# Kernel optimization log

Hardware: AMD Instinct MI355X
Metric: run time of the kernel (lower is better)

Reference implementation:

```python
import jax, jax.numpy as jnp
import numpy as np

DIM = 4096
N_HEADS = 32
N_KV_HEADS = 8
HEAD_DIM = 128
EPS = 1e-6
B, S = 1, 2048


def setup_inputs() -> dict:
    key = jax.random.key(0)
    ks = jax.random.split(key, 8)
    x = jax.random.normal(ks[0], (B, S, DIM), dtype=jnp.float32)
    # Standard RoPE cos/sin table, broadcast to (B, S, HEAD_DIM)
    inv_freq = 1.0 / (10000.0 ** (np.arange(0, HEAD_DIM, 2, dtype=np.float32) / HEAD_DIM))
    t = np.arange(S, dtype=np.float32)
    freqs = np.outer(t, inv_freq)  # (S, HEAD_DIM/2)
    emb = np.concatenate([freqs, freqs], axis=-1)  # (S, HEAD_DIM)
    cos = jnp.broadcast_to(jnp.cos(emb)[None], (B, S, HEAD_DIM))
    sin = jnp.broadcast_to(jnp.sin(emb)[None], (B, S, HEAD_DIM))
    std = 0.02
    wq = jax.random.normal(ks[1], (N_HEADS * HEAD_DIM, DIM), dtype=jnp.float32) * std
    wk = jax.random.normal(ks[2], (N_KV_HEADS * HEAD_DIM, DIM), dtype=jnp.float32) * std
    wv = jax.random.normal(ks[3], (N_KV_HEADS * HEAD_DIM, DIM), dtype=jnp.float32) * std
    wo = jax.random.normal(ks[4], (DIM, N_HEADS * HEAD_DIM), dtype=jnp.float32) * std
    q_norm_w = jnp.ones((HEAD_DIM,), dtype=jnp.float32) + 0.1 * jax.random.normal(ks[5], (HEAD_DIM,), dtype=jnp.float32)
    k_norm_w = jnp.ones((HEAD_DIM,), dtype=jnp.float32) + 0.1 * jax.random.normal(ks[6], (HEAD_DIM,), dtype=jnp.float32)
    return {"x": x, "cos": cos, "sin": sin, "wq": wq, "wk": wk, "wv": wv,
            "wo": wo, "q_norm_w": q_norm_w, "k_norm_w": k_norm_w}


def _rmsnorm(x, w):
    var = jnp.mean(jnp.square(x), axis=-1, keepdims=True)
    return x * jax.lax.rsqrt(var + EPS) * w


def _rotate_half(x):
    h = x.shape[-1] // 2
    return jnp.concatenate([-x[..., h:], x[..., :h]], axis=-1)


def reference(x, cos, sin, wq, wk, wv, wo, q_norm_w, k_norm_w):
    bs, seqlen, _ = x.shape
    # QKV projections (Linear with weight of shape (out, in), no bias)
    xq = (x @ wq.T).reshape(bs, seqlen, N_HEADS, HEAD_DIM)
    xk = (x @ wk.T).reshape(bs, seqlen, N_KV_HEADS, HEAD_DIM)
    xv = (x @ wv.T).reshape(bs, seqlen, N_KV_HEADS, HEAD_DIM)
    # QK RMSNorm (after projection, before RoPE)
    xq = _rmsnorm(xq, q_norm_w)
    xk = _rmsnorm(xk, k_norm_w)
    # RoPE: cos/sin (B, S, D) -> broadcast over head axis
    c = cos[:, :, None, :]
    s = sin[:, :, None, :]
    xq = xq * c + _rotate_half(xq) * s
    xk = xk * c + _rotate_half(xk) * s
    # GQA: repeat kv heads
    n_rep = N_HEADS // N_KV_HEADS
    xk = jnp.repeat(xk, n_rep, axis=2)
    xv = jnp.repeat(xv, n_rep, axis=2)
    # (B, H, S, D)
    q = xq.transpose(0, 2, 1, 3)
    k = xk.transpose(0, 2, 1, 3)
    v = xv.transpose(0, 2, 1, 3)
    scale = HEAD_DIM ** -0.5
    scores = jnp.einsum('bhqd,bhkd->bhqk', q, k) * scale
    causal = jnp.tril(jnp.ones((seqlen, seqlen), dtype=bool))
    scores = jnp.where(causal, scores, jnp.finfo(scores.dtype).min)
    probs = jax.nn.softmax(scores, axis=-1)
    out = jnp.einsum('bhqk,bhkd->bhqd', probs, v)
    out = out.transpose(0, 2, 1, 3).reshape(bs, seqlen, N_HEADS * HEAD_DIM)
    return out @ wo.T
```

## Files before the change

### kernel.cpp

```cpp
#include <hip/hip_runtime.h>


#define S_LEN 2048
#define DIM 4096
#define NH 32
#define NKV 8
#define HD 128
#define SCALE 0.08838834764831845f

typedef __attribute__((ext_vector_type(8))) short short8;
typedef __attribute__((ext_vector_type(4))) float f32x4;

__device__ __forceinline__ float bf2f(unsigned short u) {
  union { unsigned i; float f; } c; c.i = ((unsigned)u) << 16; return c.f;
}
__device__ __forceinline__ unsigned short f2bf(float f) {
  union { float f; unsigned u; } c; c.f = f;
  return (unsigned short)((c.u + 0x7fffu + ((c.u >> 16) & 1u)) >> 16);
}
__device__ __forceinline__ void cvt8(const float* __restrict__ g,
                                     unsigned short* __restrict__ d) {
  const float4 a = *(const float4*)g;
  const float4 b = *(const float4*)(g + 4);
  short8 p;
  p[0] = (short)f2bf(a.x); p[1] = (short)f2bf(a.y);
  p[2] = (short)f2bf(a.z); p[3] = (short)f2bf(a.w);
  p[4] = (short)f2bf(b.x); p[5] = (short)f2bf(b.y);
  p[6] = (short)f2bf(b.z); p[7] = (short)f2bf(b.w);
  *(short8*)d = p;
}
__device__ __forceinline__ void storeC(float* p, float v) { *p = v; }
__device__ __forceinline__ void storeC(unsigned short* p, float v) { *p = f2bf(v); }

#define G_X   1048576u
#define G_WQ  2097152u
#define G_WK   524288u
#define G_WV   524288u
#define G_QKV (G_WQ + G_WK + G_WV)

__global__ __launch_bounds__(256)
void cvt_all(const float* __restrict__ x,  const float* __restrict__ wq,
             const float* __restrict__ wk, const float* __restrict__ wv,
             const float* __restrict__ wo,
             unsigned short* __restrict__ xb,
             unsigned short* __restrict__ wqkvb,
             unsigned short* __restrict__ wob) {
  const size_t g = (size_t)blockIdx.x * 256 + threadIdx.x;
  if (g < G_X) {
    cvt8(x + g * 8, xb + g * 8);
  } else if (g < G_X + G_QKV) {
    const size_t o = g - G_X;
    const float* s = (o < G_WQ) ? wq + o * 8
                   : (o < G_WQ + G_WK) ? wk + (o - G_WQ) * 8
                                       : wv + (o - G_WQ - G_WK) * 8;
    cvt8(s, wqkvb + o * 8);
  } else {
    const size_t o = g - (G_X + G_QKV);
    cvt8(wo + o * 8, wob + o * 8);
  }
}

template <int QKV, typename TC>
__global__ __launch_bounds__(256)
void gemm16(const unsigned short* __restrict__ A,
            const unsigned short* __restrict__ B,
            TC* __restrict__ C0,
            unsigned short* __restrict__ Ck,
            unsigned short* __restrict__ Cv, int K) {
  __shared__ unsigned short lsA[128 * 64];
  __shared__ unsigned short lsB[128 * 64];

  const int t    = threadIdx.x;
  const int lane = t & 63;
  const int w    = t >> 6;
  const int m0   = blockIdx.y * 128;
  const int n0   = blockIdx.x * 128;

  f32x4 acc[4][4];
#pragma unroll
  for (int a = 0; a < 4; ++a)
#pragma unroll
    for (int b = 0; b < 4; ++b)
#pragma unroll
      for (int e = 0; e < 4; ++e) acc[a][b][e] = 0.f;

  const int l15  = lane & 15;
  const int qd   = lane >> 4;
  const int wr   = w >> 1, wc = w & 1;
  const int sr8  = lane >> 3;
  const int skg  = (lane & 7) ^ sr8;
  const int l7   = l15 & 7;

  const int nkb = K >> 6;
  for (int kb = 0; kb < nkb; ++kb) {
    const int k0 = kb << 6;
#pragma unroll
    for (int c = 0; c < 4; ++c) {
      const int chunk = c * 4 + w;
      const int row   = chunk * 8 + sr8;
      const unsigned short* ga = A + (size_t)(m0 + row) * K + k0 + skg * 8;
      const unsigned short* gb = B + (size_t)(n0 + row) * K + k0 + skg * 8;
      __builtin_amdgcn_global_load_lds(
          (const __attribute__((address_space(1))) void*)ga,
          (__attribute__((address_space(3))) void*)(lsA + chunk * 512), 16, 0, 0);
      __builtin_amdgcn_global_load_lds(
          (const __attribute__((address_space(1))) void*)gb,
          (__attribute__((address_space(3))) void*)(lsB + chunk * 512), 16, 0, 0);
    }
    asm volatile("s_waitcnt vmcnt(0)" ::: "memory");
    __syncthreads();

#pragma unroll
    for (int half = 0; half < 2; ++half) {
      const int kg = (half * 4 + qd) ^ l7;
      short8 af[4], bf[4];
#pragma unroll
      for (int mi = 0; mi < 4; ++mi)
        af[mi] = *(const short8*)(lsA + (wr * 64 + mi * 16 + l15) * 64 + kg * 8);
#pragma unroll
      for (int ni = 0; ni < 4; ++ni)
        bf[ni] = *(const short8*)(lsB + (wc * 64 + ni * 16 + l15) * 64 + kg * 8);
#pragma unroll
      for (int mi = 0; mi < 4; ++mi)
#pragma unroll
        for (int ni = 0; ni < 4; ++ni)
          acc[mi][ni] = __builtin_amdgcn_mfma_f32_16x16x32_bf16(
              af[mi], bf[ni], acc[mi][ni], 0, 0, 0);
    }
    __syncthreads();
  }

#pragma unroll
  for (int mi = 0; mi < 4; ++mi)
#pragma unroll
    for (int i = 0; i < 4; ++i) {
      const int grow = m0 + wr * 64 + mi * 16 + qd * 4 + i;
#pragma unroll
      for (int ni = 0; ni < 4; ++ni) {
        const int gcol = n0 + wc * 64 + ni * 16 + l15;
        if (QKV) {
          if (n0 < 4096)
            storeC((unsigned short*)C0 + (size_t)grow * 4096 + gcol,
                   acc[mi][ni][i]);
          else if (n0 < 5120)
            Ck[(size_t)grow * 1024 + (gcol - 4096)] = f2bf(acc[mi][ni][i]);
          else
            Cv[(size_t)(gcol - 5120) * S_LEN + grow] = f2bf(acc[mi][ni][i]);
        } else {
          storeC(C0 + (size_t)grow * 4096 + gcol, acc[mi][ni][i]);
        }
      }
    }
}

__global__ __launch_bounds__(512)
void norm_rope(unsigned short* __restrict__ qb, unsigned short* __restrict__ kb,
               const float* __restrict__ cosb, const float* __restrict__ sinb,
               const float* __restrict__ qw, const float* __restrict__ kw) {
  const int s    = blockIdx.x;
  const int w    = threadIdx.x >> 6;
  const int l    = threadIdx.x & 63;
  const int hh   = blockIdx.y * 8 + w;

  unsigned short* p; const float* wt;
  if (hh < NH) { p = qb + (size_t)s * (NH * HD) + hh * HD; wt = qw; }
  else         { p = kb + (size_t)s * (NKV * HD) + (hh - NH) * HD; wt = kw; }

  const float v0 = bf2f(p[l]);
  const float v1 = bf2f(p[l + 64]);
  float ss = v0 * v0 + v1 * v1;
#pragma unroll
  for (int off = 32; off; off >>= 1) ss += __shfl_xor(ss, off);
  const float r = rsqrtf(ss * (1.f / 128.f) + 1e-6f);

  const float xn0 = v0 * r * wt[l];
  const float xn1 = v1 * r * wt[l + 64];
  const float c0 = cosb[s * HD + l],      s0 = sinb[s * HD + l];
  const float c1 = cosb[s * HD + l + 64], s1 = sinb[s * HD + l + 64];
  float o0 = xn0 * c0 - xn1 * s0;
  float o1 = xn1 * c1 + xn0 * s1;
  if (hh < NH) { o0 *= SCALE; o1 *= SCALE; }
  p[l]      = f2bf(o0);
  p[l + 64] = f2bf(o1);
}

#define PSTR 72

__global__ __launch_bounds__(256)
void attn_mfma(const unsigned short* __restrict__ qB,
               const unsigned short* __restrict__ kB,
               const unsigned short* __restrict__ vT,
               unsigned short* __restrict__ oB) {
  __shared__ unsigned short ks[64 * 128];
  __shared__ unsigned short vt[128 * 64];
  __shared__ unsigned short Ps[4 * 32 * PSTR];

  const int t    = threadIdx.x;
  const int lane = t & 63;
  const int w    = t >> 6;
  const int h    = blockIdx.y;
  const int qt   = (h & 16) ? (15 - blockIdx.x) : blockIdx.x;
  const int q0   = qt * 128;
  const int kvh  = h >> 2;
  const int l15  = lane & 15;
  const int qd   = lane >> 4;
  const int l7   = l15 & 7;

  const int kr16 = lane >> 4;
  const int vr8  = lane >> 3;
  const int vkg  = (lane & 7) ^ (vr8 & 7);

  short8 qf[2][4];
#pragma unroll
  for (int f = 0; f < 2; ++f) {
    const unsigned short* qp =
        qB + (size_t)(q0 + w * 32 + f * 16 + l15) * (NH * HD) + h * HD + qd * 8;
#pragma unroll
    for (int s = 0; s < 4; ++s) qf[f][s] = *(const short8*)(qp + s * 32);
  }

  f32x4 O[2][8];
#pragma unroll
  for (int f = 0; f < 2; ++f)
#pragma unroll
    for (int nt = 0; nt < 8; ++nt)
#pragma unroll
      for (int e = 0; e < 4; ++e) O[f][nt][e] = 0.f;
  float l_i[2][4] = {{0.f, 0.f, 0.f, 0.f}, {0.f, 0.f, 0.f, 0.f}};

  unsigned short* Pw = Ps + w * (32 * PSTR);

  const int nkt = 2 * qt + 2;
  for (int kt = 0; kt < nkt; ++kt) {
#pragma unroll
    for (int c = 0; c < 4; ++c) {
      const int chunk = w * 4 + c;
      const int key = chunk * 4 + kr16;
      const int dg  = (lane & 15) ^ (key & 15);
      const unsigned short* gk = kB + (size_t)(kt * 64 + key) * (NKV * HD) +
                                 kvh * HD + dg * 8;
      __builtin_amdgcn_global_load_lds(
          (const __attribute__((address_space(1))) void*)gk,
          (__attribute__((address_space(3))) void*)(ks + chunk * 512), 16, 0, 0);
      const int dv = chunk * 8 + vr8;
      const unsigned short* gv = vT + (size_t)(kvh * HD + dv) * S_LEN +
                                 kt * 64 + vkg * 8;
      __builtin_amdgcn_global_load_lds(
          (const __attribute__((address_space(1))) void*)gv,
          (__attribute__((address_space(3))) void*)(vt + chunk * 512), 16, 0, 0);
    }
    asm volatile("s_waitcnt vmcnt(0)" ::: "memory");
    __syncthreads();

    const int dk = kt - 2 * qt;
    const bool active = (dk <= 0) || (w >= 2);
    if (active) {
      f32x4 S[2][4];
#pragma unroll
      for (int ct = 0; ct < 4; ++ct) {
#pragma unroll
        for (int e = 0; e < 4; ++e) { S[0][ct][e] = 0.f; S[1][ct][e] = 0.f; }
#pragma unroll
        for (int s = 0; s < 4; ++s) {
          const int kg = (s * 4 + qd) ^ l15;
          const short8 kf =
              *(const short8*)(ks + (ct * 16 + l15) * 128 + kg * 8);
          S[0][ct] = __builtin_amdgcn_mfma_f32_16x16x32_bf16(qf[0][s], kf,
                                                             S[0][ct], 0, 0, 0);
          S[1][ct] = __builtin_amdgcn_mfma_f32_16x16x32_bf16(qf[1][s], kf,
                                                             S[1][ct], 0, 0, 0);
        }
      }

      if (dk >= 0) {
#pragma unroll
        for (int f = 0; f < 2; ++f)
#pragma unroll
          for (int ct = 0; ct < 4; ++ct)
#pragma unroll
            for (int i = 0; i < 4; ++i) {
              const int krel = dk * 64 + ct * 16 + l15;
              const int rrel = w * 32 + f * 16 + qd * 4 + i;
              if (krel > rrel) S[f][ct][i] = -1e30f;
            }
      }

#pragma unroll
      for (int f = 0; f < 2; ++f)
#pragma unroll
        for (int ct = 0; ct < 4; ++ct)
#pragma unroll
          for (int i = 0; i < 4; ++i) {
            const float e = __expf(S[f][ct][i]);
            l_i[f][i] += e;
            Pw[(f * 16 + qd * 4 + i) * PSTR + ct * 16 + l15] = f2bf(e);
          }

      {
        short8 pf[2][2];
#pragma unroll
        for (int f = 0; f < 2; ++f) {
          pf[f][0] = *(const short8*)(Pw + (f * 16 + l15) * PSTR + qd * 8);
          pf[f][1] = *(const short8*)(Pw + (f * 16 + l15) * PSTR + 32 + qd * 8);
        }
        const int kg0 = qd ^ l7;
        const int kg1 = (4 + qd) ^ l7;
#pragma unroll
        for (int nt = 0; nt < 8; ++nt) {
          const short8 vf0 =
              *(const short8*)(vt + (nt * 16 + l15) * 64 + kg0 * 8);
          const short8 vf1 =
              *(const short8*)(vt + (nt * 16 + l15) * 64 + kg1 * 8);
          O[0][nt] = __builtin_amdgcn_mfma_f32_16x16x32_bf16(pf[0][0], vf0,
                                                             O[0][nt], 0, 0, 0);
          O[1][nt] = __builtin_amdgcn_mfma_f32_16x16x32_bf16(pf[1][0], vf0,
                                                             O[1][nt], 0, 0, 0);
          O[0][nt] = __builtin_amdgcn_mfma_f32_16x16x32_bf16(pf[0][1], vf1,
                                                             O[0][nt], 0, 0, 0);
          O[1][nt] = __builtin_amdgcn_mfma_f32_16x16x32_bf16(pf[1][1], vf1,
                                                             O[1][nt], 0, 0, 0);
        }
      }
    }
    __syncthreads();
  }

  float linv[2][4];
#pragma unroll
  for (int f = 0; f < 2; ++f)
#pragma unroll
    for (int i = 0; i < 4; ++i) {
      float s = l_i[f][i];
#pragma unroll
      for (int off = 1; off < 16; off <<= 1) s += __shfl_xor(s, off);
      linv[f][i] = 1.f / s;
    }
#pragma unroll
  for (int f = 0; f < 2; ++f)
#pragma unroll
    for (int nt = 0; nt < 8; ++nt)
#pragma unroll
      for (int i = 0; i < 4; ++i) {
        const size_t row = (size_t)(q0 + w * 32 + f * 16 + qd * 4 + i);
        oB[row * (NH * HD) + h * HD + nt * 16 + l15] =
            f2bf(O[f][nt][i] * linv[f][i]);
      }
}

extern "C" void kernel_launch(void* const* d_in, const int* in_sizes, int n_in,
                              void* d_out, int out_size, void* d_ws, size_t ws_size,
                              hipStream_t stream) {
  const float* x    = (const float*)d_in[0];
  const float* cosb = (const float*)d_in[1];
  const float* sinb = (const float*)d_in[2];
  const float* wq   = (const float*)d_in[3];
  const float* wk   = (const float*)d_in[4];
  const float* wv   = (const float*)d_in[5];
  const float* wo   = (const float*)d_in[6];
  const float* qnw  = (const float*)d_in[7];
  const float* knw  = (const float*)d_in[8];

  unsigned short* q     = (unsigned short*)d_ws;
  unsigned short* k     = q + (size_t)S_LEN * DIM;
  unsigned short* vT    = k + (size_t)S_LEN * NKV * HD;
  unsigned short* att   = vT + (size_t)NKV * HD * S_LEN;
  unsigned short* xb    = att + (size_t)S_LEN * DIM;
  unsigned short* wqkvb = xb + (size_t)S_LEN * DIM;
  unsigned short* wob   = wqkvb + (size_t)6144 * DIM;

  cvt_all<<<dim3(24576), dim3(256), 0, stream>>>(x, wq, wk, wv, wo, xb, wqkvb,
                                                 wob);
  gemm16<1, unsigned short>
      <<<dim3(48, 16), dim3(256), 0, stream>>>(xb, wqkvb, q, k, vT, DIM);
  norm_rope<<<dim3(S_LEN, 5), dim3(512), 0, stream>>>(q, k, cosb, sinb,
                                                      qnw, knw);
  attn_mfma<<<dim3(S_LEN / 128, NH), dim3(256), 0, stream>>>(q, k, vT, att);
  gemm16<0, float>
      <<<dim3(32, 16), dim3(256), 0, stream>>>(att, wob, (float*)d_out,
                                               nullptr, nullptr, DIM);
}
```

Baseline: 533.0 us.

## Double-buffer K/V tiles in attention and shrink per-wave P scratch

The attention kernel now prefetches the next K/V tile into a second LDS buffer with async global-to-LDS loads while the current tile is computed, waiting only on the older loads (vmcnt(8)) instead of draining all of them. The per-wave P buffer is halved by writing and reading back one 16-row fragment at a time, and the MFMA sections are wrapped in s_setprio raises. This is meant to hide global-load latency behind compute, at the cost of doubling K/V LDS use, which may lower occupancy. Correctness depends on the vmcnt count and the raw barriers ordering the LDS writes properly.

```diff
diff --git a/kernel.cpp b/kernel.cpp
--- a/kernel.cpp
+++ b/kernel.cpp
@@ -186,14 +186,39 @@
 
 #define PSTR 72
 
+#define STAGE_KV(KT, BUF)                                                      \
+  {                                                                            \
+    unsigned short* ksb = ks + (BUF) * 8192;                                   \
+    unsigned short* vtb = vt + (BUF) * 8192;                                   \
+    _Pragma("unroll")                                                          \
+    for (int c = 0; c < 4; ++c) {                                              \
+      const int chunk = w * 4 + c;                                             \
+      const int key = chunk * 4 + kr16;                                        \
+      const int dg  = (lane & 15) ^ (key & 15);                                \
+      const unsigned short* gk = kB + (size_t)((KT) * 64 + key) * (NKV * HD) + \
+                                 kvh * HD + dg * 8;                            \
+      __builtin_amdgcn_global_load_lds(                                        \
+          (const __attribute__((address_space(1))) void*)gk,                   \
+          (__attribute__((address_space(3))) void*)(ksb + chunk * 512),        \
+          16, 0, 0);                                                           \
+      const int dv = chunk * 8 + vr8;                                          \
+      const unsigned short* gv = vT + (size_t)(kvh * HD + dv) * S_LEN +        \
+                                 (KT) * 64 + vkg * 8;                          \
+      __builtin_amdgcn_global_load_lds(                                        \
+          (const __attribute__((address_space(1))) void*)gv,                   \
+          (__attribute__((address_space(3))) void*)(vtb + chunk * 512),        \
+          16, 0, 0);                                                           \
+    }                                                                          \
+  }
+
 __global__ __launch_bounds__(256)
 void attn_mfma(const unsigned short* __restrict__ qB,
                const unsigned short* __restrict__ kB,
                const unsigned short* __restrict__ vT,
                unsigned short* __restrict__ oB) {
-  __shared__ unsigned short ks[64 * 128];
-  __shared__ unsigned short vt[128 * 64];
-  __shared__ unsigned short Ps[4 * 32 * PSTR];
+  __shared__ unsigned short ks[2 * 64 * 128];
+  __shared__ unsigned short vt[2 * 64 * 128];
+  __shared__ unsigned short Ps[4 * 16 * PSTR];
 
   const int t    = threadIdx.x;
   const int lane = t & 63;
@@ -228,34 +253,27 @@
       for (int e = 0; e < 4; ++e) O[f][nt][e] = 0.f;
   float l_i[2][4] = {{0.f, 0.f, 0.f, 0.f}, {0.f, 0.f, 0.f, 0.f}};
 
-  unsigned short* Pw = Ps + w * (32 * PSTR);
+  unsigned short* Pw = Ps + w * (16 * PSTR);
 
   const int nkt = 2 * qt + 2;
+
+  STAGE_KV(0, 0);
+
   for (int kt = 0; kt < nkt; ++kt) {
-#pragma unroll
-    for (int c = 0; c < 4; ++c) {
-      const int chunk = w * 4 + c;
-      const int key = chunk * 4 + kr16;
-      const int dg  = (lane & 15) ^ (key & 15);
-      const unsigned short* gk = kB + (size_t)(kt * 64 + key) * (NKV * HD) +
-                                 kvh * HD + dg * 8;
-      __builtin_amdgcn_global_load_lds(
-          (const __attribute__((address_space(1))) void*)gk,
-          (__attribute__((address_space(3))) void*)(ks + chunk * 512), 16, 0, 0);
-      const int dv = chunk * 8 + vr8;
-      const unsigned short* gv = vT + (size_t)(kvh * HD + dv) * S_LEN +
-                                 kt * 64 + vkg * 8;
-      __builtin_amdgcn_global_load_lds(
-          (const __attribute__((address_space(1))) void*)gv,
-          (__attribute__((address_space(3))) void*)(vt + chunk * 512), 16, 0, 0);
-    }
-    asm volatile("s_waitcnt vmcnt(0)" ::: "memory");
-    __syncthreads();
+    const int cur = kt & 1;
+    const int kn  = (kt + 1 < nkt) ? (kt + 1) : kt;
+    STAGE_KV(kn, cur ^ 1);
+    asm volatile("s_waitcnt vmcnt(8)" ::: "memory");
+    __builtin_amdgcn_s_barrier();
+
+    const unsigned short* ksb = ks + cur * 8192;
+    const unsigned short* vtb = vt + cur * 8192;
 
     const int dk = kt - 2 * qt;
     const bool active = (dk <= 0) || (w >= 2);
     if (active) {
       f32x4 S[2][4];
+      __builtin_amdgcn_s_setprio(1);
 #pragma unroll
       for (int ct = 0; ct < 4; ++ct) {
 #pragma unroll
@@ -264,13 +282,14 @@
         for (int s = 0; s < 4; ++s) {
           const int kg = (s * 4 + qd) ^ l15;
           const short8 kf =
-              *(const short8*)(ks + (ct * 16 + l15) * 128 + kg * 8);
+              *(const short8*)(ksb + (ct * 16 + l15) * 128 + kg * 8);
           S[0][ct] = __builtin_amdgcn_mfma_f32_16x16x32_bf16(qf[0][s], kf,
                                                              S[0][ct], 0, 0, 0);
           S[1][ct] = __builtin_amdgcn_mfma_f32_16x16x32_bf16(qf[1][s], kf,
                                                              S[1][ct], 0, 0, 0);
         }
       }
+      __builtin_amdgcn_s_setprio(0);
 
       if (dk >= 0) {
 #pragma unroll
@@ -285,32 +304,31 @@
             }
       }
 
-#pragma unroll
-      for (int f = 0; f < 2; ++f)
+      short8 pf[2][2];
+#pragma unroll
+      for (int f = 0; f < 2; ++f) {
 #pragma unroll
         for (int ct = 0; ct < 4; ++ct)
 #pragma unroll
           for (int i = 0; i < 4; ++i) {
             const float e = __expf(S[f][ct][i]);
             l_i[f][i] += e;
-            Pw[(f * 16 + qd * 4 + i) * PSTR + ct * 16 + l15] = f2bf(e);
+            Pw[(qd * 4 + i) * PSTR + ct * 16 + l15] = f2bf(e);
           }
+        pf[f][0] = *(const short8*)(Pw + l15 * PSTR + qd * 8);
+        pf[f][1] = *(const short8*)(Pw + l15 * PSTR + 32 + qd * 8);
+      }
 
       {
-        short8 pf[2][2];
-#pragma unroll
-        for (int f = 0; f < 2; ++f) {
-          pf[f][0] = *(const short8*)(Pw + (f * 16 + l15) * PSTR + qd * 8);
-          pf[f][1] = *(const short8*)(Pw + (f * 16 + l15) * PSTR + 32 + qd * 8);
-        }
         const int kg0 = qd ^ l7;
         const int kg1 = (4 + qd) ^ l7;
+        __builtin_amdgcn_s_setprio(1);
 #pragma unroll
         for (int nt = 0; nt < 8; ++nt) {
           const short8 vf0 =
-              *(const short8*)(vt + (nt * 16 + l15) * 64 + kg0 * 8);
+              *(const short8*)(vtb + (nt * 16 + l15) * 64 + kg0 * 8);
           const short8 vf1 =
-              *(const short8*)(vt + (nt * 16 + l15) * 64 + kg1 * 8);
+              *(const short8*)(vtb + (nt * 16 + l15) * 64 + kg1 * 8);
           O[0][nt] = __builtin_amdgcn_mfma_f32_16x16x32_bf16(pf[0][0], vf0,
                                                              O[0][nt], 0, 0, 0);
           O[1][nt] = __builtin_amdgcn_mfma_f32_16x16x32_bf16(pf[1][0], vf0,
@@ -320,9 +338,11 @@
           O[1][nt] = __builtin_amdgcn_mfma_f32_16x16x32_bf16(pf[1][1], vf1,
                                                              O[1][nt], 0, 0, 0);
         }
+        __builtin_amdgcn_s_setprio(0);
       }
     }
-    __syncthreads();
+    __builtin_amdgcn_s_barrier();
+    __builtin_amdgcn_sched_barrier(0);
   }
 
   float linv[2][4];
```

After: 529.5 us. Within noise of the previous version (-0.7%).
